# Optimization experiments

Hardware: AMD Instinct MI355X
Metric: run time of the kernel (lower is better)

The kernel has to match this reference:

```python
import jax, jax.numpy as jnp
import numpy as np

N = 50000
E = 800000
IN_DIM, HID, OUT, DW = 128, 96, 40, 64
N_LBL = 10


def _deg_inv_sqrt(dst, n):
    # PyG gcn_norm: degree over target nodes of (A + I)
    deg = jax.ops.segment_sum(jnp.ones((dst.shape[0],), jnp.float32), dst, num_segments=n) + 1.0
    return jnp.where(deg > 0, 1.0 / jnp.sqrt(deg), 0.0)


def gcn_conv(h_in, W, b, src, dst, dinv):
    # GCNConv: out = D^-1/2 (A + I) D^-1/2 (X W) + b
    h = h_in @ W                                  # [N, F]
    norm = (dinv[src] * dinv[dst])[:, None]       # [E, 1]
    agg = jax.ops.segment_sum(h[src] * norm, dst, num_segments=h.shape[0])
    agg = agg + h * (dinv * dinv)[:, None]        # self-loop term
    return agg + b


def setup_inputs() -> dict:
    key = jax.random.key(0)
    ks = jax.random.split(key, 12)
    inp = {
        "x": jax.random.normal(ks[0], (N, IN_DIM), jnp.float32),
        "y": jax.random.uniform(ks[1], (N, OUT), jnp.float32),
        "edge_index": jax.random.randint(ks[2], (2, E), 0, N, jnp.int64 if jax.config.read("jax_enable_x64") else jnp.int32),
        "deep_walk_emb": jax.random.normal(ks[3], (N, DW), jnp.float32),
        # learned params
        "W_gcn1": jax.random.normal(ks[4], (IN_DIM, HID), jnp.float32) * (1.0 / np.sqrt(IN_DIM)),
        "b_gcn1": jnp.zeros((HID,), jnp.float32),
        "W_gcn2": jax.random.normal(ks[5], (HID, HID), jnp.float32) * (1.0 / np.sqrt(HID)),
        "b_gcn2": jnp.zeros((HID,), jnp.float32),
        "W_lbl": jax.random.normal(ks[6], (N_LBL, OUT, OUT), jnp.float32) * (1.0 / np.sqrt(OUT)),
        "b_lbl": jnp.zeros((N_LBL, OUT), jnp.float32),
        "W_fuse": jax.random.normal(ks[7], (HID + OUT + DW, OUT), jnp.float32) * (1.0 / np.sqrt(HID + OUT + DW)),
        "b_fuse": jnp.zeros((OUT,), jnp.float32),
    }
    return inp


def reference(x, y, edge_index, deep_walk_emb,
              W_gcn1, b_gcn1, W_gcn2, b_gcn2,
              W_lbl, b_lbl, W_fuse, b_fuse):
    src, dst = edge_index[0], edge_index[1]
    dinv = _deg_inv_sqrt(dst, x.shape[0])

    # feature propagation: 2 stacked GCNConv layers
    h = gcn_conv(x, W_gcn1, b_gcn1, src, dst, dinv)
    h = gcn_conv(h, W_gcn2, b_gcn2, src, dst, dinv)

    # label propagation: 10 stacked GCNConv layers via scan over stacked weights
    def step(carry, wb):
        W, b = wb
        return gcn_conv(carry, W, b, src, dst, dinv), None

    x_label, _ = jax.lax.scan(step, y, (W_lbl, b_lbl))

    fused = jnp.concatenate([h, x_label, deep_walk_emb], axis=1)  # [N, HID+OUT+DW]
    out = fused @ W_fuse + b_fuse
    return jax.nn.sigmoid(out)
```

## Files before the change

kernel.cpp:

```cpp
#include <hip/hip_runtime.h>
#include <hip/hip_bf16.h>
#include <math.h>

#define THREADS 256
typedef _Float16 h16;

__device__ __forceinline__ void ld8h(const h16* p, float* f) {
    union { uint4 u; h16 h[8]; } c;
    c.u = *(const uint4*)p;
#pragma unroll
    for (int j = 0; j < 8; ++j) f[j] = (float)c.h[j];
}

__global__ __launch_bounds__(256) void count_part_kernel(
    const int* __restrict__ dst, int* __restrict__ cnt, int E, int n)
{
    const int cls = blockIdx.x & 7;
    const int nb  = gridDim.x >> 3;
    const int sub = blockIdx.x >> 3;
    const int lo = (int)((long long)n * cls / 8);
    const int hi = (int)((long long)n * (cls + 1) / 8);
    const int stride = nb * 256;
    for (int e = sub * 256 + threadIdx.x; e < E; e += stride) {
        int d = dst[e];
        if (d >= lo && d < hi) atomicAdd(&cnt[d], 1);
    }
}

__global__ __launch_bounds__(256) void scatter_part_kernel(
    const int* __restrict__ src, const int* __restrict__ dst,
    int* __restrict__ cursor, int* __restrict__ col, int E, int n)
{
    const int cls = blockIdx.x & 7;
    const int nb  = gridDim.x >> 3;
    const int sub = blockIdx.x >> 3;
    const int lo = (int)((long long)n * cls / 8);
    const int hi = (int)((long long)n * (cls + 1) / 8);
    const int stride = nb * 256;
    for (int e = sub * 256 + threadIdx.x; e < E; e += stride) {
        int d = dst[e];
        if (d >= lo && d < hi) {
            int p = atomicAdd(&cursor[d], 1);
            col[p] = src[e];
        }
    }
}

__global__ __launch_bounds__(256) void scanp1_pre_kernel(
    const int* __restrict__ cnt, int* __restrict__ partial, int n, int NB,
    const float* __restrict__ Wl, const float* __restrict__ bl,
    const float* __restrict__ W2, const float* __restrict__ b1,
    const float* __restrict__ b2, const float* __restrict__ Wf,
    float* __restrict__ CM, float* __restrict__ betas,
    float* __restrict__ T, float* __restrict__ betaf1p, float* __restrict__ b2p)
{
    __shared__ __align__(16) float smem[13200];
    const int tid = threadIdx.x;
    const int bid = blockIdx.x;

    if (bid < NB) {
        int* red = (int*)smem;
        int base = bid * 1024 + tid * 4;
        int s = 0;
        if (base + 3 < n) {
            int4 v = *(const int4*)(cnt + base);
            s = v.x + v.y + v.z + v.w;
        } else {
            for (int k = 0; k < 4; k++) { int i = base + k; if (i < n) s += cnt[i]; }
        }
        red[tid] = s;
        __syncthreads();
        for (int off = 128; off > 0; off >>= 1) {
            if (tid < off) red[tid] += red[tid + off];
            __syncthreads();
        }
        if (tid == 0) partial[bid] = red[0];
        return;
    }

    float* Ca  = smem;
    float* Cb  = smem + 1600;
    float* sWm = smem + 3200;
    float* bls = smem + 4800;
    for (int idx = tid; idx < 100; idx += 256)
        ((float4*)bls)[idx] = ((const float4*)bl)[idx];
    for (int idx = tid; idx < 400; idx += 256)
        ((float4*)Ca)[idx] = ((const float4*)(Wf + 3840))[idx];
    __syncthreads();
    if (tid < 40) {
        float s = 0.f;
#pragma unroll
        for (int k = 0; k < 40; ++k) s = fmaf(bls[360 + k], Ca[k * 40 + tid], s);
        betas[360 + tid] = s;
    }
    __syncthreads();
    float* cur = Ca;
    float* nxt = Cb;
    for (int m = 9; m >= 0; --m) {
        for (int idx = tid; idx < 400; idx += 256)
            ((float4*)sWm)[idx] = ((const float4*)(Wl + (size_t)m * 1600))[idx];
        __syncthreads();
        for (int sid = tid; sid < 400; sid += 256) {
            int i = sid / 10, jq = sid - (sid / 10) * 10;
            const float* wr = &sWm[i * 40];
            const float4* c4 = (const float4*)cur;
            float4 a = make_float4(0.f, 0.f, 0.f, 0.f);
#pragma unroll
            for (int k = 0; k < 40; ++k) {
                float w = wr[k];
                float4 c = c4[k * 10 + jq];
                a.x = fmaf(w, c.x, a.x); a.y = fmaf(w, c.y, a.y);
                a.z = fmaf(w, c.z, a.z); a.w = fmaf(w, c.w, a.w);
            }
            ((float4*)nxt)[sid] = a;
        }
        __syncthreads();
        if (m >= 1 && tid < 40) {
            float s = 0.f;
            const float* br = &bls[(m - 1) * 40];
#pragma unroll
            for (int k = 0; k < 40; ++k) s = fmaf(br[k], nxt[k * 40 + tid], s);
            betas[(size_t)(m - 1) * 40 + tid] = s;
        }
        float* t = cur; cur = nxt; nxt = t;
        __syncthreads();
    }
    for (int idx = tid; idx < 1600; idx += 256) CM[idx] = cur[idx];
    __syncthreads();

    float* sW2  = smem;
    float* sWf1 = smem + 9216;
    float* vq   = smem + 13056;
    for (int idx = tid; idx < 2304; idx += 256)
        ((float4*)sW2)[idx] = ((const float4*)W2)[idx];
    for (int idx = tid; idx < 960; idx += 256)
        ((float4*)sWf1)[idx] = ((const float4*)Wf)[idx];
    __syncthreads();
    for (int idx = tid; idx < 3840; idx += 256) {
        int k = idx / 40, j = idx - (idx / 40) * 40;
        float s = 0.f;
#pragma unroll 8
        for (int q = 0; q < 96; ++q) s = fmaf(sW2[k * 96 + q], sWf1[q * 40 + j], s);
        T[idx] = s;
    }
    if (tid < 96) {
        float s = 0.f;
        for (int k = 0; k < 96; ++k) s = fmaf(b1[k], sW2[k * 96 + tid], s);
        vq[tid] = s;
    }
    __syncthreads();
    if (tid < 40) {
        float s1 = 0.f, s2 = 0.f;
        for (int q = 0; q < 96; ++q) {
            float w = sWf1[q * 40 + tid];
            s1 = fmaf(vq[q], w, s1);
            s2 = fmaf(b2[q], w, s2);
        }
        betaf1p[tid] = s1;
        b2p[tid] = s2;
    }
}

__global__ __launch_bounds__(256) void scanp2_wf_kernel(
    int* __restrict__ partial, int* __restrict__ rowptr, int nb, int n,
    const float* __restrict__ W1, const float* __restrict__ T, float* __restrict__ WF)
{
    __shared__ __align__(16) float smem[3840];
    const int tid = threadIdx.x;
    if (blockIdx.x == 0) {
        int* sm = (int*)smem;
        int v = (tid < nb) ? partial[tid] : 0;
        sm[tid] = v;
        __syncthreads();
        int acc = v;
        for (int off = 1; off < 256; off <<= 1) {
            int t = (tid >= off) ? sm[tid - off] : 0;
            __syncthreads();
            acc += t;
            sm[tid] = acc;
            __syncthreads();
        }
        if (tid < nb) partial[tid] = acc - v;
        if (tid == 255) rowptr[n] = sm[255];
        return;
    }
    for (int idx = tid; idx < 960; idx += 256)
        ((float4*)smem)[idx] = ((const float4*)T)[idx];
    __syncthreads();
    int idx = (blockIdx.x - 1) * 256 + tid;
    int i = idx / 40, j = idx - (idx / 40) * 40;
    float s = 0.f;
#pragma unroll 8
    for (int k = 0; k < 96; ++k) s = fmaf(W1[(size_t)i * 96 + k], smem[k * 40 + j], s);
    WF[idx] = s;
}

__global__ __launch_bounds__(256) void scan_p3(const int* __restrict__ cnt, const int* __restrict__ partial,
                                               int* __restrict__ rowptr, int* __restrict__ cursor,
                                               float* __restrict__ dinv, int n) {
    __shared__ int tsum[256];
    int tid = threadIdx.x;
    int base = blockIdx.x * 1024 + tid * 4;
    int v0 = 0, v1 = 0, v2 = 0, v3 = 0;
    if (base + 3 < n) {
        int4 t = *(const int4*)(cnt + base);
        v0 = t.x; v1 = t.y; v2 = t.z; v3 = t.w;
    } else {
        if (base + 0 < n) v0 = cnt[base + 0];
        if (base + 1 < n) v1 = cnt[base + 1];
        if (base + 2 < n) v2 = cnt[base + 2];
        if (base + 3 < n) v3 = cnt[base + 3];
    }
    int s = v0 + v1 + v2 + v3;
    tsum[tid] = s;
    __syncthreads();
    int acc = s;
    for (int off = 1; off < 256; off <<= 1) {
        int t = (tid >= off) ? tsum[tid - off] : 0;
        __syncthreads();
        acc += t;
        tsum[tid] = acc;
        __syncthreads();
    }
    int run = partial[blockIdx.x] + acc - s;
    int vv[4] = {v0, v1, v2, v3};
    for (int k = 0; k < 4; k++) {
        int i = base + k;
        if (i < n) {
            rowptr[i] = run; cursor[i] = run; run += vv[k];
            dinv[i] = rsqrtf((float)vv[k] + 1.0f);
        }
    }
}

template<int FIN, int FOUT, typename TX, typename TO, int DODINV>
__global__ __launch_bounds__(256) void gemm_kernel(
    const TX* __restrict__ X, const float* __restrict__ W,
    const float* __restrict__ dinv, TO* __restrict__ Y, int n)
{
    constexpr int KC = (FIN % 32 == 0) ? 32 : FIN;
    constexpr int NCHUNK = FIN / KC;
    constexpr int TN = (FOUT + 15) / 16;
    constexpr int FOUTP = TN * 16;
    constexpr int BM = 64;
    constexpr int KP = KC + 4;

    __shared__ __align__(16) float sX[BM * KP];
    __shared__ __align__(16) float sW[FOUTP * KP];

    const int tid = threadIdx.x;
    const int tj = tid & 15;
    const int ti = tid >> 4;
    const int i0 = blockIdx.x * BM;

    float acc[4][TN] = {};

    for (int c = 0; c < NCHUNK; ++c) {
        const int k0 = c * KC;
        __syncthreads();
        if constexpr (sizeof(TX) == 2) {
            constexpr int K8 = KC / 8;
            for (int v = tid; v < BM * K8; v += 256) {
                int r = v / K8, q = v - r * K8;
                int gi = i0 + r;
                float f[8] = {0.f, 0.f, 0.f, 0.f, 0.f, 0.f, 0.f, 0.f};
                if (gi < n) ld8h((const h16*)X + (size_t)gi * FIN + k0 + q * 8, f);
                float* p = &sX[r * KP + q * 8];
#pragma unroll
                for (int j = 0; j < 8; ++j) p[j] = f[j];
            }
        } else {
            constexpr int K4 = KC / 4;
            for (int v = tid; v < BM * K4; v += 256) {
                int r = v / K4, q = v - r * K4;
                int gi = i0 + r;
                float4 val = (gi < n) ? *(const float4*)((const float*)X + (size_t)gi * FIN + k0 + q * 4)
                                      : make_float4(0.f, 0.f, 0.f, 0.f);
                float* p = &sX[r * KP + q * 4];
                p[0] = val.x; p[1] = val.y; p[2] = val.z; p[3] = val.w;
            }
        }
        for (int v = tid; v < KC * FOUT; v += 256) {
            int kk = v / FOUT;
            int j = v - kk * FOUT;
            sW[j * KP + kk] = W[(size_t)(k0 + kk) * FOUT + j];
        }
        __syncthreads();
#pragma unroll
        for (int kk = 0; kk < KC; kk += 4) {
            float4 xv[4];
#pragma unroll
            for (int m = 0; m < 4; ++m)
                xv[m] = *(const float4*)&sX[(ti + 16 * m) * KP + kk];
#pragma unroll
            for (int u = 0; u < TN; ++u) {
                float4 wv = *(const float4*)&sW[(tj + 16 * u) * KP + kk];
#pragma unroll
                for (int m = 0; m < 4; ++m) {
                    acc[m][u] = fmaf(xv[m].x, wv.x, acc[m][u]);
                    acc[m][u] = fmaf(xv[m].y, wv.y, acc[m][u]);
                    acc[m][u] = fmaf(xv[m].z, wv.z, acc[m][u]);
                    acc[m][u] = fmaf(xv[m].w, wv.w, acc[m][u]);
                }
            }
        }
    }

#pragma unroll
    for (int m = 0; m < 4; ++m) {
        int gi = i0 + ti + 16 * m;
        if (gi >= n) continue;
        float dv = 1.f;
        if constexpr (DODINV) dv = dinv[gi];
#pragma unroll
        for (int u = 0; u < TN; ++u) {
            int j = tj + 16 * u;
            if (j < FOUT) Y[(size_t)gi * FOUT + j] = (TO)(acc[m][u] * dv);
        }
    }
}

template<int F, int MODE>
__device__ __forceinline__ void agg_body(
    const h16* __restrict__ hs, const int* __restrict__ rowptr,
    const int* __restrict__ col, const float* __restrict__ dinv,
    const float* __restrict__ bias, h16* __restrict__ out, int n,
    int bid, int tid,
    const float* __restrict__ extra32 = nullptr,
    const h16* __restrict__ f2 = nullptr,
    const float* __restrict__ bfp = nullptr,
    float* __restrict__ outf = nullptr)
{
    constexpr int F8 = F / 8;
    int gt = bid * 256 + tid;
    if (gt >= n * F8) return;
    int i = gt / F8;
    int f = gt - i * F8;
    int s = rowptr[i], e = rowptr[i + 1];
    const h16* base = hs + (size_t)f * 8;
    float acc[8];
    ld8h(hs + (size_t)i * F + f * 8, acc);
    int k = s;
    for (; k + 8 <= e; k += 8) {
        int c[8];
        union { uint4 u; h16 h[8]; } a[8];
#pragma unroll
        for (int q = 0; q < 8; ++q) c[q] = col[k + q];
#pragma unroll
        for (int q = 0; q < 8; ++q) a[q].u = *(const uint4*)(base + (size_t)c[q] * F);
#pragma unroll
        for (int j = 0; j < 8; ++j) {
            float t0 = ((float)a[0].h[j] + (float)a[1].h[j]) + ((float)a[2].h[j] + (float)a[3].h[j]);
            float t1 = ((float)a[4].h[j] + (float)a[5].h[j]) + ((float)a[6].h[j] + (float)a[7].h[j]);
            acc[j] += t0 + t1;
        }
    }
    for (; k + 4 <= e; k += 4) {
        int c0 = col[k], c1 = col[k + 1], c2 = col[k + 2], c3 = col[k + 3];
        union { uint4 u; h16 h[8]; } a0, a1, a2, a3;
        a0.u = *(const uint4*)(base + (size_t)c0 * F);
        a1.u = *(const uint4*)(base + (size_t)c1 * F);
        a2.u = *(const uint4*)(base + (size_t)c2 * F);
        a3.u = *(const uint4*)(base + (size_t)c3 * F);
#pragma unroll
        for (int j = 0; j < 8; ++j)
            acc[j] += ((float)a0.h[j] + (float)a1.h[j]) + ((float)a2.h[j] + (float)a3.h[j]);
    }
    for (; k < e; k++) {
        float v[8];
        ld8h(base + (size_t)col[k] * F, v);
#pragma unroll
        for (int j = 0; j < 8; ++j) acc[j] += v[j];
    }
    float dv = dinv[i];
    if constexpr (MODE == 3) {
        float fv[8];
        ld8h(f2 + (size_t)i * F + f * 8, fv);
        float r[8];
#pragma unroll
        for (int j = 0; j < 8; ++j) {
            float t = acc[j] * dv + bias[f * 8 + j] + fv[j] + bfp[f * 8 + j];
            r[j] = 1.f / (1.f + expf(-t));
        }
        float* po = outf + (size_t)i * F + f * 8;
        *(float4*)po       = make_float4(r[0], r[1], r[2], r[3]);
        *(float4*)(po + 4) = make_float4(r[4], r[5], r[6], r[7]);
    } else if constexpr (MODE == 2) {
        const float* pe = extra32 + (size_t)i * F + f * 8;
        float4 e0 = *(const float4*)pe;
        float4 e1 = *(const float4*)(pe + 4);
        float ex[8] = {e0.x, e0.y, e0.z, e0.w, e1.x, e1.y, e1.z, e1.w};
        union { uint4 u; h16 h[8]; } o;
#pragma unroll
        for (int j = 0; j < 8; ++j) o.h[j] = (h16)(acc[j] * dv + bias[f * 8 + j] + ex[j]);
        *(uint4*)(out + (size_t)i * F + f * 8) = o.u;
    } else {
        union { uint4 u; h16 h[8]; } o;
#pragma unroll
        for (int j = 0; j < 8; ++j) o.h[j] = (h16)((acc[j] * dv + bias[f * 8 + j]) * dv);
        *(uint4*)(out + (size_t)i * F + f * 8) = o.u;
    }
}

__global__ __launch_bounds__(256) void agg40_pre_kernel(
    const h16* __restrict__ hs, const int* __restrict__ rowptr,
    const int* __restrict__ col, const float* __restrict__ dinv,
    const float* __restrict__ bias, h16* __restrict__ out, int n) {
    agg_body<40, 1>(hs, rowptr, col, dinv, bias, out, n, blockIdx.x, threadIdx.x);
}

__global__ __launch_bounds__(256) void agg_hop1_kernel(
    const h16* __restrict__ hsA, const float* __restrict__ biasA, h16* __restrict__ outA,
    const h16* __restrict__ hsB, const float* __restrict__ biasB, h16* __restrict__ outB,
    const int* __restrict__ rowptr, const int* __restrict__ col,
    const float* __restrict__ dinv, int n, int nblkA)
{
    if (blockIdx.x < nblkA)
        agg_body<40, 1>(hsA, rowptr, col, dinv, biasA, outA, n, blockIdx.x, threadIdx.x);
    else
        agg_body<40, 1>(hsB, rowptr, col, dinv, biasB, outB, n, blockIdx.x - nblkA, threadIdx.x);
}

__global__ __launch_bounds__(256) void agg_hop2_kernel(
    const h16* __restrict__ hsA, const float* __restrict__ biasA, h16* __restrict__ outA,
    const h16* __restrict__ hsB, const float* __restrict__ biasB, h16* __restrict__ outB,
    const float* __restrict__ dw40,
    const int* __restrict__ rowptr, const int* __restrict__ col,
    const float* __restrict__ dinv, int n, int nblkA)
{
    if (blockIdx.x < nblkA)
        agg_body<40, 1>(hsA, rowptr, col, dinv, biasA, outA, n, blockIdx.x, threadIdx.x);
    else
        agg_body<40, 2>(hsB, rowptr, col, dinv, biasB, outB, n, blockIdx.x - nblkA, threadIdx.x, dw40);
}

__global__ __launch_bounds__(256) void agg_final_kernel(
    const h16* __restrict__ hs, const int* __restrict__ rowptr,
    const int* __restrict__ col, const float* __restrict__ dinv,
    const float* __restrict__ bias, const h16* __restrict__ f2,
    const float* __restrict__ bf, float* __restrict__ outf, int n)
{
    agg_body<40, 3>(hs, rowptr, col, dinv, bias, nullptr, n, blockIdx.x, threadIdx.x,
                    nullptr, f2, bf, outf);
}

extern "C" void kernel_launch(void* const* d_in, const int* in_sizes, int n_in,
                              void* d_out, int out_size, void* d_ws, size_t ws_size,
                              hipStream_t stream) {
    const float* x   = (const float*)d_in[0];
    const float* y   = (const float*)d_in[1];
    const int*   ei  = (const int*)d_in[2];
    const float* dwe = (const float*)d_in[3];
    const float* W1  = (const float*)d_in[4];
    const float* b1  = (const float*)d_in[5];
    const float* W2  = (const float*)d_in[6];
    const float* b2  = (const float*)d_in[7];
    const float* Wl  = (const float*)d_in[8];
    const float* bl  = (const float*)d_in[9];
    const float* Wf  = (const float*)d_in[10];
    const float* bf  = (const float*)d_in[11];
    float* out = (float*)d_out;

    const int n = in_sizes[0] / 128;
    const int E = in_sizes[2] / 2;
    const int* srcp = ei;
    const int* dstp = ei + E;

    char* ws = (char*)d_ws;
    size_t off = 0;
    auto alloc = [&](size_t bytes) -> void* {
        void* p = ws + off;
        off += bytes;
        off = (off + 255) & ~(size_t)255;
        return p;
    };

    int*   cnt     = (int*)alloc((size_t)n * 4);
    float* dinv    = (float*)alloc((size_t)n * 4);
    int*   rowptr  = (int*)alloc((size_t)(n + 1) * 4);
    int*   cursor  = (int*)alloc((size_t)n * 4);
    int*   partial = (int*)alloc(256 * 4);
    int*   col     = (int*)alloc((size_t)E * 4);
    h16*   Z0      = (h16*)alloc((size_t)n * 40 * 2);
    h16*   LA      = (h16*)alloc((size_t)n * 40 * 2);
    h16*   LB      = (h16*)alloc((size_t)n * 40 * 2);
    h16*   F0      = (h16*)alloc((size_t)n * 40 * 2);
    h16*   FB      = (h16*)alloc((size_t)n * 40 * 2);
    h16*   F2      = (h16*)alloc((size_t)n * 40 * 2);
    float* DW40    = (float*)alloc((size_t)n * 40 * 4);
    float* CM      = (float*)alloc(1600 * 4);
    float* betas   = (float*)alloc(10 * 40 * 4);
    float* T       = (float*)alloc(96 * 40 * 4);
    float* WF      = (float*)alloc(128 * 40 * 4);
    float* betaf1p = (float*)alloc(40 * 4);
    float* b2p     = (float*)alloc(40 * 4);
    (void)ws_size;

    const int NB      = (n + 1023) / 1024;
    const int gb_gm   = (n + 63) / 64;
    const int gb_a40  = (n * 5 + THREADS - 1) / THREADS;
    const int PART_BLOCKS = 2048;

    hipMemsetAsync(cnt, 0, (size_t)n * 4, stream);
    count_part_kernel<<<PART_BLOCKS, THREADS, 0, stream>>>(dstp, cnt, E, n);
    scanp1_pre_kernel<<<NB + 1, THREADS, 0, stream>>>(
        cnt, partial, n, NB, Wl, bl, W2, b1, b2, Wf, CM, betas, T, betaf1p, b2p);
    scanp2_wf_kernel<<<21, THREADS, 0, stream>>>(partial, rowptr, NB, n, W1, T, WF);
    scan_p3<<<NB, THREADS, 0, stream>>>(cnt, partial, rowptr, cursor, dinv, n);
    scatter_part_kernel<<<PART_BLOCKS, THREADS, 0, stream>>>(srcp, dstp, cursor, col, E, n);

    gemm_kernel<40, 40, float, h16, 1><<<gb_gm, THREADS, 0, stream>>>(y, CM, dinv, Z0, n);
    gemm_kernel<128, 40, float, h16, 1><<<gb_gm, THREADS, 0, stream>>>(x, WF, dinv, F0, n);
    gemm_kernel<64, 40, float, float, 0><<<gb_gm, THREADS, 0, stream>>>(dwe, Wf + 136 * 40, nullptr, DW40, n);

    agg_hop1_kernel<<<2 * gb_a40, THREADS, 0, stream>>>(
        Z0, betas + 0, LA, F0, betaf1p, FB, rowptr, col, dinv, n, gb_a40);
    agg_hop2_kernel<<<2 * gb_a40, THREADS, 0, stream>>>(
        LA, betas + 40, LB, FB, b2p, F2, DW40, rowptr, col, dinv, n, gb_a40);

    const h16* cur = LB;
    for (int m = 3; m <= 9; m++) {
        h16* nxt = (m & 1) ? LA : LB;
        agg40_pre_kernel<<<gb_a40, THREADS, 0, stream>>>(
            cur, rowptr, col, dinv, betas + (size_t)(m - 1) * 40, nxt, n);
        cur = nxt;
    }

    agg_final_kernel<<<gb_a40, THREADS, 0, stream>>>(
        cur, rowptr, col, dinv, betas + 9 * 40, F2, bf, out, n);
}
```

Baseline: 363.4 us.

## Parallelize weight-precompute across blocks and fold deep-walk GEMM into scan kernel

The single-block weight precompute in the scan kernel is split: one block still does the label-weight chain and bias vectors, while 15 extra blocks compute the W2·Wf1 product T in parallel, reading W2 from global memory instead of staging it in shared memory. The deep-walk embedding GEMM is moved into the scanp2 kernel as extra blocks through a shared gemm_body, removing one launch and overlapping it with the prefix-scan and WF work. The inner label-chain loop is also rewritten to load the weights as float4. This shrinks shared memory and shortens the serial critical path, at the cost of more redundant Wf loads and a larger, mixed-role kernel.

```diff
diff --git a/kernel.cpp b/kernel.cpp
--- a/kernel.cpp
+++ b/kernel.cpp
@@ -54,7 +54,7 @@
     float* __restrict__ CM, float* __restrict__ betas,
     float* __restrict__ T, float* __restrict__ betaf1p, float* __restrict__ b2p)
 {
-    __shared__ __align__(16) float smem[13200];
+    __shared__ __align__(16) float smem[5200];
     const int tid = threadIdx.x;
     const int bid = blockIdx.x;
 
@@ -78,96 +78,205 @@
         return;
     }
 
-    float* Ca  = smem;
-    float* Cb  = smem + 1600;
-    float* sWm = smem + 3200;
-    float* bls = smem + 4800;
-    for (int idx = tid; idx < 100; idx += 256)
-        ((float4*)bls)[idx] = ((const float4*)bl)[idx];
-    for (int idx = tid; idx < 400; idx += 256)
-        ((float4*)Ca)[idx] = ((const float4*)(Wf + 3840))[idx];
-    __syncthreads();
-    if (tid < 40) {
-        float s = 0.f;
-#pragma unroll
-        for (int k = 0; k < 40; ++k) s = fmaf(bls[360 + k], Ca[k * 40 + tid], s);
-        betas[360 + tid] = s;
-    }
-    __syncthreads();
-    float* cur = Ca;
-    float* nxt = Cb;
-    for (int m = 9; m >= 0; --m) {
+    if (bid == NB) {
+        float* Ca  = smem;
+        float* Cb  = smem + 1600;
+        float* sWm = smem + 3200;
+        float* bls = smem + 4800;
+        for (int idx = tid; idx < 100; idx += 256)
+            ((float4*)bls)[idx] = ((const float4*)bl)[idx];
         for (int idx = tid; idx < 400; idx += 256)
-            ((float4*)sWm)[idx] = ((const float4*)(Wl + (size_t)m * 1600))[idx];
-        __syncthreads();
-        for (int sid = tid; sid < 400; sid += 256) {
-            int i = sid / 10, jq = sid - (sid / 10) * 10;
-            const float* wr = &sWm[i * 40];
-            const float4* c4 = (const float4*)cur;
-            float4 a = make_float4(0.f, 0.f, 0.f, 0.f);
-#pragma unroll
-            for (int k = 0; k < 40; ++k) {
-                float w = wr[k];
-                float4 c = c4[k * 10 + jq];
-                a.x = fmaf(w, c.x, a.x); a.y = fmaf(w, c.y, a.y);
-                a.z = fmaf(w, c.z, a.z); a.w = fmaf(w, c.w, a.w);
+            ((float4*)Ca)[idx] = ((const float4*)(Wf + 3840))[idx];
+        __syncthreads();
+        if (tid < 40) {
+            float s = 0.f;
+#pragma unroll
+            for (int k = 0; k < 40; ++k) s = fmaf(bls[360 + k], Ca[k * 40 + tid], s);
+            betas[360 + tid] = s;
+        }
+        __syncthreads();
+        float* cur = Ca;
+        float* nxt = Cb;
+        for (int m = 9; m >= 0; --m) {
+            for (int idx = tid; idx < 400; idx += 256)
+                ((float4*)sWm)[idx] = ((const float4*)(Wl + (size_t)m * 1600))[idx];
+            __syncthreads();
+            for (int sid = tid; sid < 400; sid += 256) {
+                int i = sid / 10, jq = sid - (sid / 10) * 10;
+                const float4* wr4 = (const float4*)&sWm[i * 40];
+                const float4* c4 = (const float4*)cur;
+                float4 a = make_float4(0.f, 0.f, 0.f, 0.f);
+#pragma unroll
+                for (int k4 = 0; k4 < 10; ++k4) {
+                    float4 w = wr4[k4];
+                    float4 c0 = c4[(k4 * 4 + 0) * 10 + jq];
+                    float4 c1 = c4[(k4 * 4 + 1) * 10 + jq];
+                    float4 c2 = c4[(k4 * 4 + 2) * 10 + jq];
+                    float4 c3 = c4[(k4 * 4 + 3) * 10 + jq];
+                    a.x = fmaf(w.x, c0.x, fmaf(w.y, c1.x, fmaf(w.z, c2.x, fmaf(w.w, c3.x, a.x))));
+                    a.y = fmaf(w.x, c0.y, fmaf(w.y, c1.y, fmaf(w.z, c2.y, fmaf(w.w, c3.y, a.y))));
+                    a.z = fmaf(w.x, c0.z, fmaf(w.y, c1.z, fmaf(w.z, c2.z, fmaf(w.w, c3.z, a.z))));
+                    a.w = fmaf(w.x, c0.w, fmaf(w.y, c1.w, fmaf(w.z, c2.w, fmaf(w.w, c3.w, a.w))));
+                }
+                ((float4*)nxt)[sid] = a;
             }
-            ((float4*)nxt)[sid] = a;
-        }
-        __syncthreads();
-        if (m >= 1 && tid < 40) {
+            __syncthreads();
+            if (m >= 1 && tid < 40) {
+                float s = 0.f;
+                const float* br = &bls[(m - 1) * 40];
+#pragma unroll
+                for (int k = 0; k < 40; ++k) s = fmaf(br[k], nxt[k * 40 + tid], s);
+                betas[(size_t)(m - 1) * 40 + tid] = s;
+            }
+            float* t = cur; cur = nxt; nxt = t;
+            __syncthreads();
+        }
+        for (int idx = tid; idx < 1600; idx += 256) CM[idx] = cur[idx];
+        __syncthreads();
+
+        float* sWf1 = smem;
+        float* vq   = smem + 3840;
+        for (int q2 = tid; q2 < 960; q2 += 256)
+            ((float4*)sWf1)[q2] = ((const float4*)Wf)[q2];
+        if (tid < 96) {
             float s = 0.f;
-            const float* br = &bls[(m - 1) * 40];
-#pragma unroll
-            for (int k = 0; k < 40; ++k) s = fmaf(br[k], nxt[k * 40 + tid], s);
-            betas[(size_t)(m - 1) * 40 + tid] = s;
-        }
-        float* t = cur; cur = nxt; nxt = t;
-        __syncthreads();
-    }
-    for (int idx = tid; idx < 1600; idx += 256) CM[idx] = cur[idx];
-    __syncthreads();
-
-    float* sW2  = smem;
-    float* sWf1 = smem + 9216;
-    float* vq   = smem + 13056;
-    for (int idx = tid; idx < 2304; idx += 256)
-        ((float4*)sW2)[idx] = ((const float4*)W2)[idx];
-    for (int idx = tid; idx < 960; idx += 256)
-        ((float4*)sWf1)[idx] = ((const float4*)Wf)[idx];
-    __syncthreads();
-    for (int idx = tid; idx < 3840; idx += 256) {
+            for (int k = 0; k < 96; ++k) s = fmaf(b1[k], W2[(size_t)k * 96 + tid], s);
+            vq[tid] = s;
+        }
+        __syncthreads();
+        if (tid < 40) {
+            float s1 = 0.f, s2 = 0.f;
+            for (int q = 0; q < 96; ++q) {
+                float w = sWf1[q * 40 + tid];
+                s1 = fmaf(vq[q], w, s1);
+                s2 = fmaf(b2[q], w, s2);
+            }
+            betaf1p[tid] = s1;
+            b2p[tid] = s2;
+        }
+        return;
+    }
+
+    {
+        int tb = bid - NB - 1;
+        int idx = tb * 256 + tid;
+        float* sWf1 = smem;
+        for (int q2 = tid; q2 < 960; q2 += 256)
+            ((float4*)sWf1)[q2] = ((const float4*)Wf)[q2];
+        __syncthreads();
         int k = idx / 40, j = idx - (idx / 40) * 40;
         float s = 0.f;
 #pragma unroll 8
-        for (int q = 0; q < 96; ++q) s = fmaf(sW2[k * 96 + q], sWf1[q * 40 + j], s);
+        for (int q = 0; q < 96; ++q) s = fmaf(W2[(size_t)k * 96 + q], sWf1[q * 40 + j], s);
         T[idx] = s;
     }
-    if (tid < 96) {
-        float s = 0.f;
-        for (int k = 0; k < 96; ++k) s = fmaf(b1[k], sW2[k * 96 + tid], s);
-        vq[tid] = s;
-    }
-    __syncthreads();
-    if (tid < 40) {
-        float s1 = 0.f, s2 = 0.f;
-        for (int q = 0; q < 96; ++q) {
-            float w = sWf1[q * 40 + tid];
-            s1 = fmaf(vq[q], w, s1);
-            s2 = fmaf(b2[q], w, s2);
-        }
-        betaf1p[tid] = s1;
-        b2p[tid] = s2;
-    }
-}
-
-__global__ __launch_bounds__(256) void scanp2_wf_kernel(
+}
+
+template<int FIN, int FOUT, typename TX, typename TO, int DODINV>
+__device__ __forceinline__ void gemm_body(
+    const TX* __restrict__ X, const float* __restrict__ W,
+    const float* __restrict__ dinv, TO* __restrict__ Y, int n,
+    float* sX, float* sW, int bid, int tid)
+{
+    constexpr int KC = (FIN % 32 == 0) ? 32 : FIN;
+    constexpr int NCHUNK = FIN / KC;
+    constexpr int TN = (FOUT + 15) / 16;
+    constexpr int BM = 64;
+    constexpr int KP = KC + 4;
+
+    const int tj = tid & 15;
+    const int ti = tid >> 4;
+    const int i0 = bid * BM;
+
+    float acc[4][TN] = {};
+
+    for (int c = 0; c < NCHUNK; ++c) {
+        const int k0 = c * KC;
+        __syncthreads();
+        if constexpr (sizeof(TX) == 2) {
+            constexpr int K8 = KC / 8;
+            for (int v = tid; v < BM * K8; v += 256) {
+                int r = v / K8, q = v - r * K8;
+                int gi = i0 + r;
+                float f[8] = {0.f, 0.f, 0.f, 0.f, 0.f, 0.f, 0.f, 0.f};
+                if (gi < n) ld8h((const h16*)X + (size_t)gi * FIN + k0 + q * 8, f);
+                float* p = &sX[r * KP + q * 8];
+#pragma unroll
+                for (int j = 0; j < 8; ++j) p[j] = f[j];
+            }
+        } else {
+            constexpr int K4 = KC / 4;
+            for (int v = tid; v < BM * K4; v += 256) {
+                int r = v / K4, q = v - r * K4;
+                int gi = i0 + r;
+                float4 val = (gi < n) ? *(const float4*)((const float*)X + (size_t)gi * FIN + k0 + q * 4)
+                                      : make_float4(0.f, 0.f, 0.f, 0.f);
+                float* p = &sX[r * KP + q * 4];
+                p[0] = val.x; p[1] = val.y; p[2] = val.z; p[3] = val.w;
+            }
+        }
+        for (int v = tid; v < KC * FOUT; v += 256) {
+            int kk = v / FOUT;
+            int j = v - kk * FOUT;
+            sW[j * KP + kk] = W[(size_t)(k0 + kk) * FOUT + j];
+        }
+        __syncthreads();
+#pragma unroll
+        for (int kk = 0; kk < KC; kk += 4) {
+            float4 xv[4];
+#pragma unroll
+            for (int m = 0; m < 4; ++m)
+                xv[m] = *(const float4*)&sX[(ti + 16 * m) * KP + kk];
+#pragma unroll
+            for (int u = 0; u < TN; ++u) {
+                float4 wv = *(const float4*)&sW[(tj + 16 * u) * KP + kk];
+#pragma unroll
+                for (int m = 0; m < 4; ++m) {
+                    acc[m][u] = fmaf(xv[m].x, wv.x, acc[m][u]);
+                    acc[m][u] = fmaf(xv[m].y, wv.y, acc[m][u]);
+                    acc[m][u] = fmaf(xv[m].z, wv.z, acc[m][u]);
+                    acc[m][u] = fmaf(xv[m].w, wv.w, acc[m][u]);
+                }
+            }
+        }
+    }
+
+#pragma unroll
+    for (int m = 0; m < 4; ++m) {
+        int gi = i0 + ti + 16 * m;
+        if (gi >= n) continue;
+        float dv = 1.f;
+        if constexpr (DODINV) dv = dinv[gi];
+#pragma unroll
+        for (int u = 0; u < TN; ++u) {
+            int j = tj + 16 * u;
+            if (j < FOUT) Y[(size_t)gi * FOUT + j] = (TO)(acc[m][u] * dv);
+        }
+    }
+}
+
+template<int FIN, int FOUT, typename TX, typename TO, int DODINV>
+__global__ __launch_bounds__(256) void gemm_kernel(
+    const TX* __restrict__ X, const float* __restrict__ W,
+    const float* __restrict__ dinv, TO* __restrict__ Y, int n)
+{
+    constexpr int KC = (FIN % 32 == 0) ? 32 : FIN;
+    constexpr int KP = KC + 4;
+    constexpr int TN = (FOUT + 15) / 16;
+    __shared__ __align__(16) float smem[64 * KP + TN * 16 * KP];
+    gemm_body<FIN, FOUT, TX, TO, DODINV>(X, W, dinv, Y, n, smem, smem + 64 * KP,
+                                         blockIdx.x, threadIdx.x);
+}
+
+__global__ __launch_bounds__(256) void scanp2_wf_dw_kernel(
     int* __restrict__ partial, int* __restrict__ rowptr, int nb, int n,
-    const float* __restrict__ W1, const float* __restrict__ T, float* __restrict__ WF)
-{
-    __shared__ __align__(16) float smem[3840];
+    const float* __restrict__ W1, const float* __restrict__ T, float* __restrict__ WF,
+    const float* __restrict__ dwe, const float* __restrict__ Wfbot, float* __restrict__ DW40)
+{
+    __shared__ __align__(16) float smem[4032];
     const int tid = threadIdx.x;
-    if (blockIdx.x == 0) {
+    const int bid = blockIdx.x;
+    if (bid == 0) {
         int* sm = (int*)smem;
         int v = (tid < nb) ? partial[tid] : 0;
         sm[tid] = v;
@@ -184,15 +293,20 @@
         if (tid == 255) rowptr[n] = sm[255];
         return;
     }
-    for (int idx = tid; idx < 960; idx += 256)
-        ((float4*)smem)[idx] = ((const float4*)T)[idx];
-    __syncthreads();
-    int idx = (blockIdx.x - 1) * 256 + tid;
-    int i = idx / 40, j = idx - (idx / 40) * 40;
-    float s = 0.f;
+    if (bid <= 20) {
+        for (int idx = tid; idx < 960; idx += 256)
+            ((float4*)smem)[idx] = ((const float4*)T)[idx];
+        __syncthreads();
+        int idx = (bid - 1) * 256 + tid;
+        int i = idx / 40, j = idx - (idx / 40) * 40;
+        float s = 0.f;
 #pragma unroll 8
-    for (int k = 0; k < 96; ++k) s = fmaf(W1[(size_t)i * 96 + k], smem[k * 40 + j], s);
-    WF[idx] = s;
+        for (int k = 0; k < 96; ++k) s = fmaf(W1[(size_t)i * 96 + k], smem[k * 40 + j], s);
+        WF[idx] = s;
+        return;
+    }
+    gemm_body<64, 40, float, float, 0>(dwe, Wfbot, nullptr, DW40, n,
+                                       smem, smem + 2304, bid - 21, tid);
 }
 
 __global__ __launch_bounds__(256) void scan_p3(const int* __restrict__ cnt, const int* __restrict__ partial,
@@ -229,93 +343,6 @@
         if (i < n) {
             rowptr[i] = run; cursor[i] = run; run += vv[k];
             dinv[i] = rsqrtf((float)vv[k] + 1.0f);
-        }
-    }
-}
-
-template<int FIN, int FOUT, typename TX, typename TO, int DODINV>
-__global__ __launch_bounds__(256) void gemm_kernel(
-    const TX* __restrict__ X, const float* __restrict__ W,
-    const float* __restrict__ dinv, TO* __restrict__ Y, int n)
-{
-    constexpr int KC = (FIN % 32 == 0) ? 32 : FIN;
-    constexpr int NCHUNK = FIN / KC;
-    constexpr int TN = (FOUT + 15) / 16;
-    constexpr int FOUTP = TN * 16;
-    constexpr int BM = 64;
-    constexpr int KP = KC + 4;
-
-    __shared__ __align__(16) float sX[BM * KP];
-    __shared__ __align__(16) float sW[FOUTP * KP];
-
-    const int tid = threadIdx.x;
-    const int tj = tid & 15;
-    const int ti = tid >> 4;
-    const int i0 = blockIdx.x * BM;
-
-    float acc[4][TN] = {};
-
-    for (int c = 0; c < NCHUNK; ++c) {
-        const int k0 = c * KC;
-        __syncthreads();
-        if constexpr (sizeof(TX) == 2) {
-            constexpr int K8 = KC / 8;
-            for (int v = tid; v < BM * K8; v += 256) {
-                int r = v / K8, q = v - r * K8;
-                int gi = i0 + r;
-                float f[8] = {0.f, 0.f, 0.f, 0.f, 0.f, 0.f, 0.f, 0.f};
-                if (gi < n) ld8h((const h16*)X + (size_t)gi * FIN + k0 + q * 8, f);
-                float* p = &sX[r * KP + q * 8];
-#pragma unroll
-                for (int j = 0; j < 8; ++j) p[j] = f[j];
-            }
-        } else {
-            constexpr int K4 = KC / 4;
-            for (int v = tid; v < BM * K4; v += 256) {
-                int r = v / K4, q = v - r * K4;
-                int gi = i0 + r;
-                float4 val = (gi < n) ? *(const float4*)((const float*)X + (size_t)gi * FIN + k0 + q * 4)
-                                      : make_float4(0.f, 0.f, 0.f, 0.f);
-                float* p = &sX[r * KP + q * 4];
-                p[0] = val.x; p[1] = val.y; p[2] = val.z; p[3] = val.w;
-            }
-        }
-        for (int v = tid; v < KC * FOUT; v += 256) {
-            int kk = v / FOUT;
-            int j = v - kk * FOUT;
-            sW[j * KP + kk] = W[(size_t)(k0 + kk) * FOUT + j];
-        }
-        __syncthreads();
-#pragma unroll
-        for (int kk = 0; kk < KC; kk += 4) {
-            float4 xv[4];
-#pragma unroll
-            for (int m = 0; m < 4; ++m)
-                xv[m] = *(const float4*)&sX[(ti + 16 * m) * KP + kk];
-#pragma unroll
-            for (int u = 0; u < TN; ++u) {
-                float4 wv = *(const float4*)&sW[(tj + 16 * u) * KP + kk];
-#pragma unroll
-                for (int m = 0; m < 4; ++m) {
-                    acc[m][u] = fmaf(xv[m].x, wv.x, acc[m][u]);
-                    acc[m][u] = fmaf(xv[m].y, wv.y, acc[m][u]);
-                    acc[m][u] = fmaf(xv[m].z, wv.z, acc[m][u]);
-                    acc[m][u] = fmaf(xv[m].w, wv.w, acc[m][u]);
-                }
-            }
-        }
-    }
-
-#pragma unroll
-    for (int m = 0; m < 4; ++m) {
-        int gi = i0 + ti + 16 * m;
-        if (gi >= n) continue;
-        float dv = 1.f;
-        if constexpr (DODINV) dv = dinv[gi];
-#pragma unroll
-        for (int u = 0; u < TN; ++u) {
-            int j = tj + 16 * u;
-            if (j < FOUT) Y[(size_t)gi * FOUT + j] = (TO)(acc[m][u] * dv);
         }
     }
 }
@@ -503,15 +530,15 @@
 
     hipMemsetAsync(cnt, 0, (size_t)n * 4, stream);
     count_part_kernel<<<PART_BLOCKS, THREADS, 0, stream>>>(dstp, cnt, E, n);
-    scanp1_pre_kernel<<<NB + 1, THREADS, 0, stream>>>(
+    scanp1_pre_kernel<<<NB + 16, THREADS, 0, stream>>>(
         cnt, partial, n, NB, Wl, bl, W2, b1, b2, Wf, CM, betas, T, betaf1p, b2p);
-    scanp2_wf_kernel<<<21, THREADS, 0, stream>>>(partial, rowptr, NB, n, W1, T, WF);
+    scanp2_wf_dw_kernel<<<21 + gb_gm, THREADS, 0, stream>>>(
+        partial, rowptr, NB, n, W1, T, WF, dwe, Wf + 136 * 40, DW40);
     scan_p3<<<NB, THREADS, 0, stream>>>(cnt, partial, rowptr, cursor, dinv, n);
     scatter_part_kernel<<<PART_BLOCKS, THREADS, 0, stream>>>(srcp, dstp, cursor, col, E, n);
 
     gemm_kernel<40, 40, float, h16, 1><<<gb_gm, THREADS, 0, stream>>>(y, CM, dinv, Z0, n);
     gemm_kernel<128, 40, float, h16, 1><<<gb_gm, THREADS, 0, stream>>>(x, WF, dinv, F0, n);
-    gemm_kernel<64, 40, float, float, 0><<<gb_gm, THREADS, 0, stream>>>(dwe, Wf + 136 * 40, nullptr, DW40, n);
 
     agg_hop1_kernel<<<2 * gb_a40, THREADS, 0, stream>>>(
         Z0, betas + 0, LA, F0, betaf1p, FB, rowptr, col, dinv, n, gb_a40);
```

Result: faster. 345.8 us, median of 3 (-4.8%).
